# Kernel tuning notes

Measured on AMD Instinct MI355X. Metric: run time of the kernel, lower is better.

The kernel has to match this reference:

```python
import jax, jax.numpy as jnp
import numpy as np

B, N, D, H = 32, 1024, 512, 8

def setup_inputs() -> dict:
    key = jax.random.key(0)
    ks = jax.random.split(key, 11)
    std = D ** (-0.5)
    inp = {
        'k': jax.random.normal(ks[0], (B, N, D), jnp.float32),
        'v': jax.random.normal(ks[1], (B, N, D), jnp.float32),
        'q': jax.random.normal(ks[2], (B, N, D), jnp.float32),
        # per-head Linear weights, torch layout (out, in), stacked over heads
        'Wk': jax.random.normal(ks[3], (H, D, D), jnp.float32) * std,
        'bk': jax.random.uniform(ks[4], (H, D), jnp.float32, -std, std),
        'Wv': jax.random.normal(ks[5], (H, D, D), jnp.float32) * std,
        'bv': jax.random.uniform(ks[6], (H, D), jnp.float32, -std, std),
        'Wq': jax.random.normal(ks[7], (H, D, D), jnp.float32) * std,
        'bq': jax.random.uniform(ks[8], (H, D), jnp.float32, -std, std),
        # output projection: (hidden, n_heads*hidden)
        'Wo': jax.random.normal(ks[9], (D, H * D), jnp.float32) * (H * D) ** (-0.5),
        'bo': jax.random.uniform(ks[10], (D,), jnp.float32, -(H * D) ** (-0.5), (H * D) ** (-0.5)),
    }
    return inp

def reference(k, v, q, Wk, bk, Wv, bv, Wq, bq, Wo, bo):
    # Batched per-head projections (torch Linear: y = x @ W.T + b)
    kh = jnp.einsum('bnd,hed->bhne', k, Wk) + bk[:, None, :]  # [B,H,N,D]
    vh = jnp.einsum('bnd,hed->bhne', v, Wv) + bv[:, None, :]
    qh = jnp.einsum('bnd,hed->bhne', q, Wq) + bq[:, None, :]
    scale = jnp.asarray(qh.shape[-1] ** 0.5, qh.dtype)
    scores = jnp.einsum('bhjd,bhid->bhij', kh, qh) / scale      # [B,H,Nq,Nk]
    w = jax.nn.softmax(scores, axis=-1)
    out = jnp.einsum('bhij,bhjd->bhid', w, vh)                  # [B,H,Nq,D]
    # torch stacks heads on last dim then flattens: out[..., d, h] -> d*H + h
    cat = out.transpose(0, 2, 3, 1).reshape(out.shape[0], out.shape[2], -1)  # [B,Nq,D*H]
    rep = cat @ Wo.T + bo                                        # [B,Nq,D]
    return rep
```

## Files before the change

kernel.cpp:

```cpp
#include <hip/hip_runtime.h>
#include <hip/hip_bf16.h>
#include <cstdint>
#include <type_traits>

constexpr int B_SZ = 32;
constexpr int N_SZ = 1024;
constexpr int D_SZ = 512;
constexpr int H_SZ = 8;
constexpr int HD   = H_SZ * D_SZ;

typedef __attribute__((ext_vector_type(8))) short short8;
typedef __attribute__((ext_vector_type(4))) float floatx4;
typedef unsigned short u16;
typedef unsigned int   u32;

static __device__ __forceinline__ u16 f2bf(float f) {
    union { float f; unsigned int i; } c; c.f = f;
    unsigned int x = c.i;
    unsigned int r = x + 0x7FFFu + ((x >> 16) & 1u);
    return (u16)(r >> 16);
}

static __device__ __forceinline__ u32 cvt_pk_bf16(float a, float b) {
    u32 r;
    asm("v_cvt_pk_bf16_f32 %0, %1, %2" : "=v"(r) : "v"(a), "v"(b));
    return r;
}

static __device__ __forceinline__ void ld2lds16(const u16* g, u16* l) {
    __builtin_amdgcn_global_load_lds(
        (const __attribute__((address_space(1))) void*)g,
        (__attribute__((address_space(3))) void*)l, 16, 0, 0);
}

__global__ void cvt_kernel(const float* __restrict__ src, u16* __restrict__ dst) {
    int idx = (blockIdx.x * 256 + threadIdx.x) * 4;
    float4 v = *(const float4*)(src + idx);
    ushort4 o;
    o.x = f2bf(v.x); o.y = f2bf(v.y); o.z = f2bf(v.z); o.w = f2bf(v.w);
    *(ushort4*)(dst + idx) = o;
}

__global__ void woperm_kernel(const float* __restrict__ Wo, u16* __restrict__ Wp) {
    int idx = blockIdx.x * 256 + threadIdx.x;
    int e = idx >> 12;
    int c = idx & 4095;
    int d  = c & 511;
    int hh = c >> 9;
    Wp[idx] = f2bf(Wo[((size_t)e << 12) + d * H_SZ + hh]);
}

template<int OM>
__global__ __launch_bounds__(256, 2)
void gemm_bt(const u16* __restrict__ A, const u16* __restrict__ W,
             const float* __restrict__ bias, void* __restrict__ Cout,
             int M, int Nc, int K)
{
    __shared__ u16 Alds[2][128 * 32];
    __shared__ u16 Blds[2][128 * 32];
    const int tid  = threadIdx.x;
    const int lane = tid & 63;
    const int wave = tid >> 6;
    const int wm = wave >> 1, wn = wave & 1;
    const int m16 = lane & 15, quad = lane >> 4;

    const int nbx = gridDim.x;
    const int nwg = nbx * (int)gridDim.y;
    const int wg  = (int)blockIdx.x + (int)blockIdx.y * nbx;
    const int swz = (wg & 7) * (nwg >> 3) + (wg >> 3);
    const int bx  = swz % nbx;
    const int by  = swz / nbx;
    const size_t tm0 = (size_t)bx * 128;
    const size_t tn0 = (size_t)by * 128;

    floatx4 acc[4][4];
#pragma unroll
    for (int i = 0; i < 4; i++)
#pragma unroll
        for (int j = 0; j < 4; j++) acc[i][j] = (floatx4){0.f, 0.f, 0.f, 0.f};

    const int srow = lane >> 2;
    const int scol = (lane & 3) * 8;
    const u16* ag0 = A + (tm0 + wave * 32 + srow) * (size_t)K + scol;
    const u16* ag1 = ag0 + (size_t)16 * K;
    const u16* bg0 = W + (tn0 + wave * 32 + srow) * (size_t)K + scol;
    const u16* bg1 = bg0 + (size_t)16 * K;

    const int nT = K >> 5;

#define STAGE(t, buf)                                            \
    do {                                                         \
        size_t ko = (size_t)(t) * 32;                            \
        u16* al = &Alds[(buf)][wave * 1024];                     \
        u16* bl = &Blds[(buf)][wave * 1024];                     \
        ld2lds16(ag0 + ko, al);                                  \
        ld2lds16(ag1 + ko, al + 512);                            \
        ld2lds16(bg0 + ko, bl);                                  \
        ld2lds16(bg1 + ko, bl + 512);                            \
    } while (0)

    STAGE(0, 0);
    for (int t = 0; t < nT; ++t) {
        __syncthreads();
        if (t + 1 < nT) STAGE(t + 1, (t + 1) & 1);
        const u16* Ab = Alds[t & 1];
        const u16* Bb = Blds[t & 1];
        short8 af[4], bf[4];
#pragma unroll
        for (int i = 0; i < 4; i++) {
            af[i] = *(const short8*)&Ab[(wm * 64 + i * 16 + m16) * 32 + quad * 8];
            bf[i] = *(const short8*)&Bb[(wn * 64 + i * 16 + m16) * 32 + quad * 8];
        }
#pragma unroll
        for (int i = 0; i < 4; i++)
#pragma unroll
            for (int j = 0; j < 4; j++)
                acc[i][j] = __builtin_amdgcn_mfma_f32_16x16x32_bf16(af[i], bf[j], acc[i][j], 0, 0, 0);
    }
#undef STAGE

#pragma unroll
    for (int j = 0; j < 4; j++) {
        int col = (int)tn0 + wn * 64 + j * 16 + m16;
        float bsv = bias[col];
#pragma unroll
        for (int i = 0; i < 4; i++) {
            size_t row = tm0 + wm * 64 + i * 16 + quad * 4;
            if constexpr (OM == 2) {
                int cloc = (int)(row >> 10);
                int n0   = (int)(row & 1023);
                ushort4 pk;
                pk.x = f2bf(acc[i][j][0] + bsv);
                pk.y = f2bf(acc[i][j][1] + bsv);
                pk.z = f2bf(acc[i][j][2] + bsv);
                pk.w = f2bf(acc[i][j][3] + bsv);
                u16* vtp = (u16*)Cout;
                *(ushort4*)&vtp[((size_t)cloc * HD + col) * N_SZ + n0] = pk;
            } else {
#pragma unroll
                for (int r = 0; r < 4; r++) {
                    if constexpr (OM == 1)
                        ((float*)Cout)[(row + r) * (size_t)Nc + col] = acc[i][j][r] + bsv;
                    else
                        ((u16*)Cout)[(row + r) * (size_t)Nc + col] = f2bf(acc[i][j][r] + bsv);
                }
            }
        }
    }
}

__global__ __launch_bounds__(256, 2)
void attn_kernel(const u16* __restrict__ qh, const u16* __restrict__ kh,
                 const u16* __restrict__ vt, u16* __restrict__ ao)
{
    __shared__ u16 Klds[32 * 512];
    __shared__ u16 Vtlds[512 * 32];
    u16*   Pov    = Klds;
    float* alphaF = (float*)&Klds[2560];
    float* lF     = (float*)&Klds[2688];
    u32*   flagp  = (u32*)&Klds[2816];

    const int tid  = threadIdx.x;
    const int lane = tid & 63;
    const int wave = tid >> 6;
    const int m16  = lane & 15;
    const int quad = lane >> 4;

    const int orig = blockIdx.x + ((int)blockIdx.y << 4) + ((int)blockIdx.z << 7);
    const int cpx  = ((int)gridDim.z << 7) >> 3;
    const int swz  = (orig & 7) * cpx + (orig >> 3);
    const int qt = swz & 15;
    const int h  = (swz >> 4) & 7;
    const int bb = swz >> 7;

    const int kxor = m16 & 7;
    const int qx8  = (quad ^ (kxor & 3)) * 8;
    const int kx32 = (kxor & 4) * 8;
    const u16* kaddrE = &Klds[m16 * 512 + qx8 + kx32];
    const u16* kaddrO = &Klds[m16 * 512 + qx8 - kx32];
    const int vx8 = (quad ^ (m16 & 3) ^ ((m16 >> 2) & 3)) * 8;
    const u16* vaddr = &Vtlds[m16 * 32 + vx8];
    const int ebase = wave * 16 + (lane >> 2);
    const int cw8   = ((lane & 3) ^ ((lane >> 2) & 3) ^ ((lane >> 4) & 3)) * 8;

    const int qrow = qt * 64 + wave * 16 + m16;
    const u16* qptr = qh + ((size_t)(bb * N_SZ + qrow)) * HD + h * D_SZ + quad * 8;
    short8 qfrag[16];
#pragma unroll
    for (int kk = 0; kk < 16; kk++)
        qfrag[kk] = *(const short8*)(qptr + kk * 32);

    floatx4 acc[8][4];
#pragma unroll
    for (int j = 0; j < 8; j++)
#pragma unroll
        for (int qc = 0; qc < 4; qc++) acc[j][qc] = (floatx4){0.f, 0.f, 0.f, 0.f};

    float mrow = -3.0e38f, lrow = 0.f;

    const float scale = 0.04419417382415922f;
    const u16* kbase  = kh + ((size_t)(bb * N_SZ)) * HD + h * D_SZ;
    const u16* vtbase = vt + ((size_t)bb * HD + h * D_SZ) * N_SZ;

    short8 kreg[8];
#pragma unroll
    for (int i = 0; i < 8; i++) {
        int row = i * 4 + wave;
        kreg[i] = *(const short8*)(kbase + (size_t)row * HD + lane * 8);
    }

    for (int kt = 0; kt < 32; kt++) {
        __syncthreads();
#pragma unroll
        for (int i = 0; i < 8; i++) {
            int row = i * 4 + wave;
            int cp  = lane ^ (row & 7);
            *(short8*)&Klds[row * 512 + cp * 8] = kreg[i];
        }
        __syncthreads();

        short8 vreg[8];
#pragma unroll
        for (int i = 0; i < 8; i++) {
            int e = i * 64 + ebase;
            vreg[i] = *(const short8*)(vtbase + (size_t)e * N_SZ + kt * 32 + (lane & 3) * 8);
        }

        floatx4 s0a = (floatx4){0.f,0.f,0.f,0.f}, s0b = s0a, s1a = s0a, s1b = s0a;
        __builtin_amdgcn_s_setprio(1);
#pragma unroll
        for (int kk = 0; kk < 16; kk++) {
            const u16* p = (kk & 1) ? kaddrO : kaddrE;
            short8 kb0 = *(const short8*)(p + kk * 32);
            short8 kb1 = *(const short8*)(p + kk * 32 + 8192);
            if (kk & 1) {
                s0b = __builtin_amdgcn_mfma_f32_16x16x32_bf16(kb0, qfrag[kk], s0b, 0, 0, 0);
                s1b = __builtin_amdgcn_mfma_f32_16x16x32_bf16(kb1, qfrag[kk], s1b, 0, 0, 0);
            } else {
                s0a = __builtin_amdgcn_mfma_f32_16x16x32_bf16(kb0, qfrag[kk], s0a, 0, 0, 0);
                s1a = __builtin_amdgcn_mfma_f32_16x16x32_bf16(kb1, qfrag[kk], s1a, 0, 0, 0);
            }
        }
        __builtin_amdgcn_s_setprio(0);
        floatx4 s0 = s0a + s0b;
        floatx4 s1 = s1a + s1b;

        float a[8];
#pragma unroll
        for (int r = 0; r < 4; r++) { a[r] = s0[r] * scale; a[4 + r] = s1[r] * scale; }
        float pm = fmaxf(fmaxf(fmaxf(a[0], a[1]), fmaxf(a[2], a[3])),
                         fmaxf(fmaxf(a[4], a[5]), fmaxf(a[6], a[7])));
        pm = fmaxf(pm, __shfl_xor(pm, 16, 64));
        pm = fmaxf(pm, __shfl_xor(pm, 32, 64));
        float alpha = 1.0f;
        u32 wflag = 0u;
        if (__any(pm > mrow + 8.0f)) {
            float mnew = fmaxf(mrow, pm);
            alpha = __expf(mrow - mnew);
            mrow = mnew;
            wflag = 1u;
        }
        float p[8];
        float ps = 0.f;
#pragma unroll
        for (int i = 0; i < 8; i++) { p[i] = __expf(a[i] - mrow); ps += p[i]; }
        ps += __shfl_xor(ps, 16, 64);
        ps += __shfl_xor(ps, 32, 64);
        lrow = lrow * alpha + ps;

        u32 w0 = cvt_pk_bf16(p[0], p[1]);
        u32 w1 = cvt_pk_bf16(p[2], p[3]);
        u32 w2 = cvt_pk_bf16(p[4], p[5]);
        u32 w3 = cvt_pk_bf16(p[6], p[7]);

        int ktn = (kt < 31) ? (kt + 1) : kt;
#pragma unroll
        for (int i = 0; i < 8; i++) {
            int row = i * 4 + wave;
            kreg[i] = *(const short8*)(kbase + (size_t)(ktn * 32 + row) * HD + lane * 8);
        }

        __syncthreads();

#pragma unroll
        for (int i = 0; i < 8; i++) {
            int e = i * 64 + ebase;
            *(short8*)&Vtlds[e * 32 + cw8] = vreg[i];
        }
        {
            int q40 = (wave * 16 + m16) * 40;
            uint2 lo; lo.x = w0; lo.y = w1;
            uint2 hi; hi.x = w2; hi.y = w3;
            *(uint2*)&Pov[q40 + quad * 4]      = lo;
            *(uint2*)&Pov[q40 + 16 + quad * 4] = hi;
        }
        if (quad == 0) alphaF[wave * 16 + m16] = alpha;
        if (lane == 0) flagp[wave] = wflag;
        __syncthreads();

        u32 f = flagp[0] | flagp[1] | flagp[2] | flagp[3];
        if (f) {
#pragma unroll
            for (int qc = 0; qc < 4; qc++) {
#pragma unroll
                for (int r = 0; r < 4; r++) {
                    float av = alphaF[qc * 16 + quad * 4 + r];
#pragma unroll
                    for (int j = 0; j < 8; j++) acc[j][qc][r] *= av;
                }
            }
        }

        short8 pf[4];
#pragma unroll
        for (int qc = 0; qc < 4; qc++)
            pf[qc] = *(const short8*)&Pov[(qc * 16 + m16) * 40 + quad * 8];
        __builtin_amdgcn_s_setprio(1);
#pragma unroll
        for (int j = 0; j < 8; j++) {
            short8 vf = *(const short8*)(vaddr + (wave * 8 + j) * 512);
#pragma unroll
            for (int qc = 0; qc < 4; qc++)
                acc[j][qc] = __builtin_amdgcn_mfma_f32_16x16x32_bf16(pf[qc], vf, acc[j][qc], 0, 0, 0);
        }
        __builtin_amdgcn_s_setprio(0);
    }

    if (quad == 0) lF[wave * 16 + m16] = lrow;
    __syncthreads();
#pragma unroll
    for (int qc = 0; qc < 4; qc++) {
#pragma unroll
        for (int r = 0; r < 4; r++) {
            int row = qt * 64 + qc * 16 + quad * 4 + r;
            float invl = 1.0f / lF[qc * 16 + quad * 4 + r];
            size_t obase = ((size_t)(bb * N_SZ + row)) * HD + h * D_SZ + wave * 128;
#pragma unroll
            for (int j = 0; j < 8; j++)
                ao[obase + j * 16 + m16] = f2bf(acc[j][qc][r] * invl);
        }
    }
}

extern "C" void kernel_launch(void* const* d_in, const int* in_sizes, int n_in,
                              void* d_out, int out_size, void* d_ws, size_t ws_size,
                              hipStream_t stream)
{
    const float* kin = (const float*)d_in[0];
    const float* vin = (const float*)d_in[1];
    const float* qin = (const float*)d_in[2];
    const float* Wk  = (const float*)d_in[3];
    const float* bk  = (const float*)d_in[4];
    const float* Wv  = (const float*)d_in[5];
    const float* bv  = (const float*)d_in[6];
    const float* Wq  = (const float*)d_in[7];
    const float* bq  = (const float*)d_in[8];
    const float* Wo  = (const float*)d_in[9];
    const float* bo  = (const float*)d_in[10];
    float* out = (float*)d_out;

    u16* ws = (u16*)d_ws;
    const size_t wEl      = (size_t)H_SZ * D_SZ * D_SZ;
    const size_t permEl   = (size_t)D_SZ * HD;
    const size_t inEl     = (size_t)N_SZ * D_SZ;
    const size_t perBatch = (size_t)N_SZ * HD;
    const size_t fixedEl  = 3 * wEl + permEl;
    const size_t perB     = 4 * perBatch + 3 * inEl;
    long long availEl = (long long)(ws_size / 2) - (long long)fixedEl;
    int C = 1;
    if (availEl > 0) {
        long long c = availEl / (long long)perB;
        C = (int)(c < 1 ? 1 : (c > B_SZ ? B_SZ : c));
    }

    u16* wqb = ws;
    u16* wkb = wqb + wEl;
    u16* wvb = wkb + wEl;
    u16* wop = wvb + wEl;
    u16* qcb = wop + permEl;
    u16* kcb = qcb + (size_t)C * inEl;
    u16* vcb = kcb + (size_t)C * inEl;
    u16* qh  = vcb + (size_t)C * inEl;
    u16* khb = qh  + (size_t)C * perBatch;
    u16* vtb = khb + (size_t)C * perBatch;
    u16* ao  = vtb + (size_t)C * perBatch;

    const int cvtBlocks = (int)(wEl / 1024);
    cvt_kernel<<<cvtBlocks, 256, 0, stream>>>(Wq, wqb);
    cvt_kernel<<<cvtBlocks, 256, 0, stream>>>(Wk, wkb);
    cvt_kernel<<<cvtBlocks, 256, 0, stream>>>(Wv, wvb);
    woperm_kernel<<<(int)(permEl / 256), 256, 0, stream>>>(Wo, wop);

    for (int b0 = 0; b0 < B_SZ; b0 += C) {
        int Cc = (B_SZ - b0 < C) ? (B_SZ - b0) : C;
        int M = Cc * N_SZ;
        int cvB = (int)((size_t)Cc * inEl / 1024);
        cvt_kernel<<<cvB, 256, 0, stream>>>(qin + (size_t)b0 * inEl, qcb);
        cvt_kernel<<<cvB, 256, 0, stream>>>(kin + (size_t)b0 * inEl, kcb);
        cvt_kernel<<<cvB, 256, 0, stream>>>(vin + (size_t)b0 * inEl, vcb);
        dim3 gp(M / 128, HD / 128);
        gemm_bt<0><<<gp, 256, 0, stream>>>(qcb, wqb, bq, qh,  M, HD, D_SZ);
        gemm_bt<0><<<gp, 256, 0, stream>>>(kcb, wkb, bk, khb, M, HD, D_SZ);
        gemm_bt<2><<<gp, 256, 0, stream>>>(vcb, wvb, bv, vtb, M, HD, D_SZ);
        attn_kernel<<<dim3(N_SZ / 64, H_SZ, Cc), 256, 0, stream>>>(qh, khb, vtb, ao);
        gemm_bt<1><<<dim3(M / 128, D_SZ / 128), 256, 0, stream>>>(ao, wop, bo,
                                                                  out + (size_t)b0 * N_SZ * D_SZ, M, D_SZ, HD);
    }
}
```

Measured before the change: 3.113 ms.

## Split-K output projection with separate reduction and single-buffered GEMM LDS

The output projection GEMM (K=4096) is split into four K slices along a third grid dimension. Each slice writes fp32 partials to workspace, and a new reduce kernel sums them and adds the bias. The aim is more workgroups and shorter K loops for the narrow N=512 projection. The GEMM also drops LDS double buffering in favour of a load-sync-compute pattern and raises launch bounds to 3 blocks per CU. The cost is extra partial-sum traffic, one more launch, less load/compute overlap in every GEMM, and workspace growth that may shrink the batch chunk size C.

```diff
diff --git a/kernel.cpp b/kernel.cpp
--- a/kernel.cpp
+++ b/kernel.cpp
@@ -50,29 +50,51 @@
     Wp[idx] = f2bf(Wo[((size_t)e << 12) + d * H_SZ + hh]);
 }
 
+__global__ void reduce_kernel(const float* __restrict__ part, const float* __restrict__ bo,
+                              float* __restrict__ out, int Mtot) {
+    int idx = (blockIdx.x * 256 + threadIdx.x) * 4;
+    size_t plane = (size_t)Mtot * 512;
+    float4 s0 = *(const float4*)(part + idx);
+    float4 s1 = *(const float4*)(part + plane + idx);
+    float4 s2 = *(const float4*)(part + 2 * plane + idx);
+    float4 s3 = *(const float4*)(part + 3 * plane + idx);
+    float4 b  = *(const float4*)(bo + (idx & 511));
+    float4 r;
+    r.x = s0.x + s1.x + s2.x + s3.x + b.x;
+    r.y = s0.y + s1.y + s2.y + s3.y + b.y;
+    r.z = s0.z + s1.z + s2.z + s3.z + b.z;
+    r.w = s0.w + s1.w + s2.w + s3.w + b.w;
+    *(float4*)(out + idx) = r;
+}
+
 template<int OM>
-__global__ __launch_bounds__(256, 2)
+__global__ __launch_bounds__(256, 3)
 void gemm_bt(const u16* __restrict__ A, const u16* __restrict__ W,
              const float* __restrict__ bias, void* __restrict__ Cout,
-             int M, int Nc, int K)
+             int M, int Nc, int K, int lda, int ldw)
 {
-    __shared__ u16 Alds[2][128 * 32];
-    __shared__ u16 Blds[2][128 * 32];
+    __shared__ u16 Alds[128 * 32];
+    __shared__ u16 Blds[128 * 32];
     const int tid  = threadIdx.x;
     const int lane = tid & 63;
     const int wave = tid >> 6;
     const int wm = wave >> 1, wn = wave & 1;
     const int m16 = lane & 15, quad = lane >> 4;
 
-    const int nbx = gridDim.x;
-    const int nwg = nbx * (int)gridDim.y;
-    const int wg  = (int)blockIdx.x + (int)blockIdx.y * nbx;
+    const int nbx = gridDim.x, nby = gridDim.y;
+    const int nwg = nbx * nby * (int)gridDim.z;
+    const int wg  = (int)blockIdx.x + nbx * ((int)blockIdx.y + nby * (int)blockIdx.z);
     const int swz = (wg & 7) * (nwg >> 3) + (wg >> 3);
     const int bx  = swz % nbx;
-    const int by  = swz / nbx;
+    const int t1  = swz / nbx;
+    const int by  = t1 % nby;
+    const int kz  = t1 / nby;
     const size_t tm0 = (size_t)bx * 128;
     const size_t tn0 = (size_t)by * 128;
 
+    const u16* Ak = A + (size_t)kz * K;
+    const u16* Wk = W + (size_t)kz * K;
+
     floatx4 acc[4][4];
 #pragma unroll
     for (int i = 0; i < 4; i++)
@@ -81,35 +103,30 @@
 
     const int srow = lane >> 2;
     const int scol = (lane & 3) * 8;
-    const u16* ag0 = A + (tm0 + wave * 32 + srow) * (size_t)K + scol;
-    const u16* ag1 = ag0 + (size_t)16 * K;
-    const u16* bg0 = W + (tn0 + wave * 32 + srow) * (size_t)K + scol;
-    const u16* bg1 = bg0 + (size_t)16 * K;
+    const u16* ag0 = Ak + (tm0 + wave * 32 + srow) * (size_t)lda + scol;
+    const u16* ag1 = ag0 + (size_t)16 * lda;
+    const u16* bg0 = Wk + (tn0 + wave * 32 + srow) * (size_t)ldw + scol;
+    const u16* bg1 = bg0 + (size_t)16 * ldw;
 
     const int nT = K >> 5;
 
-#define STAGE(t, buf)                                            \
-    do {                                                         \
-        size_t ko = (size_t)(t) * 32;                            \
-        u16* al = &Alds[(buf)][wave * 1024];                     \
-        u16* bl = &Blds[(buf)][wave * 1024];                     \
-        ld2lds16(ag0 + ko, al);                                  \
-        ld2lds16(ag1 + ko, al + 512);                            \
-        ld2lds16(bg0 + ko, bl);                                  \
-        ld2lds16(bg1 + ko, bl + 512);                            \
-    } while (0)
-
-    STAGE(0, 0);
     for (int t = 0; t < nT; ++t) {
         __syncthreads();
-        if (t + 1 < nT) STAGE(t + 1, (t + 1) & 1);
-        const u16* Ab = Alds[t & 1];
-        const u16* Bb = Blds[t & 1];
+        {
+            size_t ko = (size_t)t * 32;
+            u16* al = &Alds[wave * 1024];
+            u16* bl = &Blds[wave * 1024];
+            ld2lds16(ag0 + ko, al);
+            ld2lds16(ag1 + ko, al + 512);
+            ld2lds16(bg0 + ko, bl);
+            ld2lds16(bg1 + ko, bl + 512);
+        }
+        __syncthreads();
         short8 af[4], bf[4];
 #pragma unroll
         for (int i = 0; i < 4; i++) {
-            af[i] = *(const short8*)&Ab[(wm * 64 + i * 16 + m16) * 32 + quad * 8];
-            bf[i] = *(const short8*)&Bb[(wn * 64 + i * 16 + m16) * 32 + quad * 8];
+            af[i] = *(const short8*)&Alds[(wm * 64 + i * 16 + m16) * 32 + quad * 8];
+            bf[i] = *(const short8*)&Blds[(wn * 64 + i * 16 + m16) * 32 + quad * 8];
         }
 #pragma unroll
         for (int i = 0; i < 4; i++)
@@ -117,12 +134,11 @@
             for (int j = 0; j < 4; j++)
                 acc[i][j] = __builtin_amdgcn_mfma_f32_16x16x32_bf16(af[i], bf[j], acc[i][j], 0, 0, 0);
     }
-#undef STAGE
 
 #pragma unroll
     for (int j = 0; j < 4; j++) {
         int col = (int)tn0 + wn * 64 + j * 16 + m16;
-        float bsv = bias[col];
+        float bsv = (OM == 3) ? 0.f : bias[col];
 #pragma unroll
         for (int i = 0; i < 4; i++) {
             size_t row = tm0 + wm * 64 + i * 16 + quad * 4;
@@ -136,6 +152,11 @@
                 pk.w = f2bf(acc[i][j][3] + bsv);
                 u16* vtp = (u16*)Cout;
                 *(ushort4*)&vtp[((size_t)cloc * HD + col) * N_SZ + n0] = pk;
+            } else if constexpr (OM == 3) {
+                float* pout = (float*)Cout + (size_t)kz * M * Nc;
+#pragma unroll
+                for (int r = 0; r < 4; r++)
+                    pout[(row + r) * (size_t)Nc + col] = acc[i][j][r];
             } else {
 #pragma unroll
                 for (int r = 0; r < 4; r++) {
@@ -365,7 +386,7 @@
     const size_t inEl     = (size_t)N_SZ * D_SZ;
     const size_t perBatch = (size_t)N_SZ * HD;
     const size_t fixedEl  = 3 * wEl + permEl;
-    const size_t perB     = 4 * perBatch + 3 * inEl;
+    const size_t perB     = 4 * perBatch + 3 * inEl + 8 * inEl;
     long long availEl = (long long)(ws_size / 2) - (long long)fixedEl;
     int C = 1;
     if (availEl > 0) {
@@ -384,6 +405,7 @@
     u16* khb = qh  + (size_t)C * perBatch;
     u16* vtb = khb + (size_t)C * perBatch;
     u16* ao  = vtb + (size_t)C * perBatch;
+    float* part = (float*)(ao + (size_t)C * perBatch);
 
     const int cvtBlocks = (int)(wEl / 1024);
     cvt_kernel<<<cvtBlocks, 256, 0, stream>>>(Wq, wqb);
@@ -398,12 +420,14 @@
         cvt_kernel<<<cvB, 256, 0, stream>>>(qin + (size_t)b0 * inEl, qcb);
         cvt_kernel<<<cvB, 256, 0, stream>>>(kin + (size_t)b0 * inEl, kcb);
         cvt_kernel<<<cvB, 256, 0, stream>>>(vin + (size_t)b0 * inEl, vcb);
-        dim3 gp(M / 128, HD / 128);
-        gemm_bt<0><<<gp, 256, 0, stream>>>(qcb, wqb, bq, qh,  M, HD, D_SZ);
-        gemm_bt<0><<<gp, 256, 0, stream>>>(kcb, wkb, bk, khb, M, HD, D_SZ);
-        gemm_bt<2><<<gp, 256, 0, stream>>>(vcb, wvb, bv, vtb, M, HD, D_SZ);
+        dim3 gp(M / 128, HD / 128, 1);
+        gemm_bt<0><<<gp, 256, 0, stream>>>(qcb, wqb, bq, qh,  M, HD, D_SZ, D_SZ, D_SZ);
+        gemm_bt<0><<<gp, 256, 0, stream>>>(kcb, wkb, bk, khb, M, HD, D_SZ, D_SZ, D_SZ);
+        gemm_bt<2><<<gp, 256, 0, stream>>>(vcb, wvb, bv, vtb, M, HD, D_SZ, D_SZ, D_SZ);
         attn_kernel<<<dim3(N_SZ / 64, H_SZ, Cc), 256, 0, stream>>>(qh, khb, vtb, ao);
-        gemm_bt<1><<<dim3(M / 128, D_SZ / 128), 256, 0, stream>>>(ao, wop, bo,
-                                                                  out + (size_t)b0 * N_SZ * D_SZ, M, D_SZ, HD);
-    }
-}
+        gemm_bt<3><<<dim3(M / 128, D_SZ / 128, 4), 256, 0, stream>>>(
+            ao, wop, bo, part, M, D_SZ, HD / 4, HD, HD);
+        reduce_kernel<<<(M * D_SZ) / 1024, 256, 0, stream>>>(
+            part, bo, out + (size_t)b0 * N_SZ * D_SZ, M);
+    }
+}
```

New measurement: 3.127 ms. No clear change (+0.4%).
